# Kernel optimization log

Measured on AMD Instinct MI355X. Metric: run time of the kernel, lower is better.

## Reference

```python
import jax, jax.numpy as jnp
import numpy as np

D_MODEL = 1024
NUM_HEADS = 16
D_K = D_MODEL // NUM_HEADS  # 64


def setup_inputs() -> dict:
    key = jax.random.key(0)
    ks = jax.random.split(key, 12)
    B, S = 4, 2048
    scale = 1.0 / np.sqrt(D_MODEL)
    inp = {
        'query': jax.random.normal(ks[0], (B, S, D_MODEL), jnp.float32),
        'key': jax.random.normal(ks[1], (B, S, D_MODEL), jnp.float32),
        'value': jax.random.normal(ks[2], (B, S, D_MODEL), jnp.float32),
        # per-head projection weights stacked along head axis [H, d_model, d_k]
        'Wq': jax.random.normal(ks[3], (NUM_HEADS, D_MODEL, D_K), jnp.float32) * scale,
        'bq': jax.random.normal(ks[4], (NUM_HEADS, D_K), jnp.float32) * 0.01,
        'Wk': jax.random.normal(ks[5], (NUM_HEADS, D_MODEL, D_K), jnp.float32) * scale,
        'bk': jax.random.normal(ks[6], (NUM_HEADS, D_K), jnp.float32) * 0.01,
        'Wv': jax.random.normal(ks[7], (NUM_HEADS, D_MODEL, D_K), jnp.float32) * scale,
        'bv': jax.random.normal(ks[8], (NUM_HEADS, D_K), jnp.float32) * 0.01,
        'Wo': jax.random.normal(ks[9], (NUM_HEADS * D_K, D_MODEL), jnp.float32) * scale,
        'bo': jax.random.normal(ks[10], (D_MODEL,), jnp.float32) * 0.01,
    }
    return inp


def reference(query, key, value, Wq, bq, Wk, bk, Wv, bv, Wo, bo):
    # Per-head linear projections, batched over heads: [B,S,D] x [H,D,K] -> [B,H,S,K]
    q = jnp.einsum('bsd,hdk->bhsk', query, Wq) + bq[None, :, None, :]
    k = jnp.einsum('bsd,hdk->bhsk', key, Wk) + bk[None, :, None, :]
    v = jnp.einsum('bsd,hdk->bhsk', value, Wv) + bv[None, :, None, :]
    # Scaled dot-product attention per head
    scores = jnp.einsum('bhqk,bhsk->bhqs', q, k) / jnp.sqrt(jnp.asarray(D_K, q.dtype))
    attn = jax.nn.softmax(scores, axis=-1)
    heads = jnp.einsum('bhqs,bhsk->bhqk', attn, v)  # [B,H,S,K]
    # Concat heads -> [B,S,H*K], then output projection
    B, H, S, K = heads.shape
    concat = jnp.transpose(heads, (0, 2, 1, 3)).reshape(B, S, H * K)
    return concat @ Wo + bo
```

## Files before the change

kernel.cpp:

```cpp
#include <hip/hip_runtime.h>
#include <hip/hip_bf16.h>

typedef __bf16 bf16_t;
typedef __bf16 bf16x8 __attribute__((ext_vector_type(8)));
typedef __bf16 bf16x4 __attribute__((ext_vector_type(4)));
typedef float f32x4 __attribute__((ext_vector_type(4)));
typedef float f32x16 __attribute__((ext_vector_type(16)));

constexpr int BB = 4;
constexpr int SS = 2048;
constexpr int DM = 1024;
constexpr int NH = 16;
constexpr int DK = 64;
constexpr int MROWS = BB * SS;

template <int N> struct IC { static constexpr int V = N; };

__device__ inline uint32_t pkbf16(float a, float b) {
    union { bf16_t h[2]; uint32_t u; } x;
    x.h[0] = (bf16_t)a; x.h[1] = (bf16_t)b;
    return x.u;
}

__device__ inline float fexp2(float x) { return __builtin_amdgcn_exp2f(x); }

__device__ inline void gld16(const bf16_t* g, bf16_t* l) {
    __builtin_amdgcn_global_load_lds((const __attribute__((address_space(1))) void*)g,
                                     (__attribute__((address_space(3))) void*)l, 16, 0, 0);
}

__device__ inline f32x16 mfma32(bf16x8 a, bf16x8 b, f32x16 c) {
    return __builtin_amdgcn_mfma_f32_32x32x16_bf16(a, b, c, 0, 0, 0);
}

__device__ inline bf16x8 lds_rd(const bf16_t* base, int row, int slot) {
    return *(const bf16x8*)((const char*)base + row * 128 + ((slot ^ (row & 7)) << 4));
}

constexpr float QSCALE = (float)(1.4426950408889634 / 8.0);

__global__ __launch_bounds__(256) void k_prepw(const float* __restrict__ Wq,
                                               const float* __restrict__ Wk,
                                               const float* __restrict__ Wv,
                                               const float* __restrict__ Wo,
                                               bf16_t* __restrict__ Wt,
                                               bf16_t* __restrict__ Wot) {
    __shared__ float tile[32][33];
    const int bid = blockIdx.x;
    const int tx = threadIdx.x & 31, ty = threadIdx.x >> 5;
    if (bid < 3072) {
        const int zz = bid >> 6;
        const int r = bid & 63;
        const int cb = (r & 1) * 32, rb = (r >> 1) * 32;
        const int zt = zz >> 4, zh = zz & 15;
        const float* src = (zt == 0) ? Wq : ((zt == 1) ? Wk : Wv);
        const float sc = (zt == 0) ? QSCALE : 1.0f;
        const long zoff = (long)zh * DM * DK;
        bf16_t* d = Wt + (size_t)zt * DM * DM + (size_t)zh * DK * DM;
#pragma unroll
        for (int i = 0; i < 4; ++i) {
            int rr = rb + ty + i * 8;
            tile[ty + i * 8][tx] = src[zoff + (long)rr * DK + cb + tx];
        }
        __syncthreads();
#pragma unroll
        for (int i = 0; i < 4; ++i) {
            int c = cb + ty + i * 8;
            d[(long)c * DM + rb + tx] = (bf16_t)(tile[tx][ty + i * 8] * sc);
        }
    } else {
        const int idx = bid - 3072;
        const int cb = (idx & 31) * 32, rb = (idx >> 5) * 32;
#pragma unroll
        for (int i = 0; i < 4; ++i) {
            int rr = rb + ty + i * 8;
            tile[ty + i * 8][tx] = Wo[(long)rr * DM + cb + tx];
        }
        __syncthreads();
#pragma unroll
        for (int i = 0; i < 4; ++i) {
            int c = cb + ty + i * 8;
            Wot[(long)c * DM + rb + tx] = (bf16_t)tile[tx][ty + i * 8];
        }
    }
}

__global__ __launch_bounds__(256) void k_proj(
    const float* __restrict__ Aq, const float* __restrict__ Ak, const float* __restrict__ Av,
    const bf16_t* __restrict__ Wt,
    const float* __restrict__ bq, const float* __restrict__ bk, const float* __restrict__ bv,
    bf16_t* __restrict__ qkv) {
    const int hwid = blockIdx.x;
    const int c = hwid & 7, j = hwid >> 3;
    const int z = j >> 6;
    const int r = j & 63;
    const int n0 = (r & 7) * 128;
    const int m0 = (c * 8 + (r >> 3)) * 128;

    const float* A = (z == 0) ? Aq : ((z == 1) ? Ak : Av);
    const float* bias = (z == 0) ? bq : ((z == 1) ? bk : bv);
    const float bscale = (z == 0) ? QSCALE : 1.0f;
    const bf16_t* Bt = Wt + (size_t)z * DM * DM;
    bf16_t* outp = qkv + (size_t)z * BB * NH * SS * DK;

    __shared__ __align__(16) union SM {
        struct { bf16_t a[2][128][72]; bf16_t b[2][8192]; } s;
        bf16_t vt[128][136];
    } sm;

    const int t = threadIdx.x;
    const int lane = t & 63, w = t >> 6;
    const int lr = lane & 15, lg = lane >> 4;
    const int wr = w >> 1, wc = w & 1;

    f32x4 acc[4][4] = {};
    float4 apf[8];

    const int brow = t >> 3, bssl = t & 7;
    const size_t bsrc = (size_t)(n0 + brow) * DM + ((bssl ^ (brow & 7)) << 3);
    const int ar0 = t >> 4, aseg = t & 15;

#pragma unroll
    for (int p = 0; p < 4; ++p)
        gld16(&Bt[bsrc + p * 32 * DM], &sm.s.b[0][(p * 256 + w * 64) * 8]);
#pragma unroll
    for (int p = 0; p < 8; ++p)
        apf[p] = *(const float4*)&A[(size_t)(m0 + ar0 + p * 16) * DM + aseg * 4];
#pragma unroll
    for (int p = 0; p < 8; ++p) {
        bf16x4 pk = {(bf16_t)apf[p].x, (bf16_t)apf[p].y, (bf16_t)apf[p].z, (bf16_t)apf[p].w};
        *(bf16x4*)&sm.s.a[0][ar0 + p * 16][aseg * 4] = pk;
    }
    __syncthreads();

    auto body = [&](auto icur, int kt) {
        constexpr int cur = decltype(icur)::V;
        const int k1 = (kt + 1) * 64;
        if (kt + 1 < 16) {
#pragma unroll
            for (int p = 0; p < 4; ++p)
                gld16(&Bt[bsrc + k1 + p * 32 * DM], &sm.s.b[cur ^ 1][(p * 256 + w * 64) * 8]);
#pragma unroll
            for (int p = 0; p < 8; ++p)
                apf[p] = *(const float4*)&A[(size_t)(m0 + ar0 + p * 16) * DM + k1 + aseg * 4];
        }
#pragma unroll
        for (int ks = 0; ks < 2; ++ks) {
            const int lk = ks * 32 + lg * 8;
            bf16x8 af[4], bfm[4];
#pragma unroll
            for (int i = 0; i < 4; ++i) af[i] = *(const bf16x8*)&sm.s.a[cur][wr * 64 + i * 16 + lr][lk];
#pragma unroll
            for (int jj = 0; jj < 4; ++jj) bfm[jj] = lds_rd(sm.s.b[cur], wc * 64 + jj * 16 + lr, ks * 4 + lg);
#pragma unroll
            for (int i = 0; i < 4; ++i)
#pragma unroll
                for (int jj = 0; jj < 4; ++jj)
                    acc[i][jj] = __builtin_amdgcn_mfma_f32_16x16x32_bf16(af[i], bfm[jj], acc[i][jj], 0, 0, 0);
        }
        if (kt + 1 < 16) {
#pragma unroll
            for (int p = 0; p < 8; ++p) {
                bf16x4 pk = {(bf16_t)apf[p].x, (bf16_t)apf[p].y, (bf16_t)apf[p].z, (bf16_t)apf[p].w};
                *(bf16x4*)&sm.s.a[cur ^ 1][ar0 + p * 16][aseg * 4] = pk;
            }
        }
        __syncthreads();
    };

#pragma unroll 1
    for (int kt = 0; kt < 16; kt += 2) {
        body(IC<0>{}, kt);
        body(IC<1>{}, kt + 1);
    }

    const int b = m0 >> 11, s0 = m0 & (SS - 1);
    if (z == 2) {
#pragma unroll
        for (int i = 0; i < 4; ++i)
#pragma unroll
            for (int jj = 0; jj < 4; ++jj) {
                int col = wc * 64 + jj * 16 + lr;
                float bv_ = bias[n0 + col];
#pragma unroll
                for (int rr = 0; rr < 4; ++rr)
                    sm.vt[col][wr * 64 + i * 16 + lg * 4 + rr] = (bf16_t)(acc[i][jj][rr] + bv_);
            }
        __syncthreads();
#pragma unroll
        for (int pp = 0; pp < 8; ++pp) {
            int d = pp * 16 + (t >> 4);
            int cs = (t & 15) * 8;
            bf16x8 v = *(const bf16x8*)&sm.vt[d][cs];
            int h = (n0 + d) >> 6, dd = d & 63;
            *(bf16x8*)&outp[((size_t)(b * NH + h) * DK + dd) * SS + s0 + cs] = v;
        }
    } else {
#pragma unroll
        for (int i = 0; i < 4; ++i) {
#pragma unroll
            for (int jj = 0; jj < 4; ++jj) {
                int col = wc * 64 + jj * 16 + lr;
                int h = (n0 + col) >> 6, ko = col & 63;
                float bv_ = bias[n0 + col] * bscale;
#pragma unroll
                for (int rr = 0; rr < 4; ++rr) {
                    int s = s0 + wr * 64 + i * 16 + lg * 4 + rr;
                    outp[(((size_t)b * NH + h) * SS + s) * DK + ko] = (bf16_t)(acc[i][jj][rr] + bv_);
                }
            }
        }
    }
}

__global__ __launch_bounds__(256, 2) void k_attn(const bf16_t* __restrict__ qkv,
                                                 bf16_t* __restrict__ concat) {
    const int hw = blockIdx.x;
    const int lb = (hw & 7) * 64 + (hw >> 3);
    const int qt = lb & 7;
    const int h = (lb >> 3) & 15;
    const int b = lb >> 7;

    const size_t PH = (size_t)BB * NH * SS * DK;
    const bf16_t* qp = qkv + ((size_t)(b * NH + h) * SS) * DK;
    const bf16_t* kp = qp + PH;
    const bf16_t* vtp = qkv + 2 * PH + (size_t)(b * NH + h) * DK * SS;

    __shared__ __align__(16) bf16_t k_lds[2][4096];
    __shared__ __align__(16) bf16_t v_lds[2][4096];

    const int t = threadIdx.x;
    const int lane = t & 63, w = t >> 6;
    const int l31 = lane & 31;
    const bool hf = (lane >> 5) != 0;

    const int sr = t >> 3, ssl = t & 7;
    const int prow = (sr & ~12) | ((sr & 4) << 1) | ((sr & 8) >> 1);
    const int ssw = (ssl ^ (sr & 7)) * 8;
    const size_t okA = (size_t)prow * DK + ssw;
    const size_t ovA = (size_t)sr * SS + ssw;

    const int qbase = qt * 256 + w * 64;
    bf16x8 qf0[4], qf1[4];
#pragma unroll
    for (int ks = 0; ks < 4; ++ks) {
        qf0[ks] = *(const bf16x8*)&qp[(size_t)(qbase + l31) * DK + ks * 16 + (hf ? 8 : 0)];
        qf1[ks] = *(const bf16x8*)&qp[(size_t)(qbase + 32 + l31) * DK + ks * 16 + (hf ? 8 : 0)];
    }

    f32x16 oa00 = {}, oa01 = {}, oa10 = {}, oa11 = {};
    float lsum0 = 0.f, lsum1 = 0.f;
    f32x16 zc = {};
    asm volatile("" : "+v"(zc));

    constexpr int NT = SS / 64;

    gld16(kp + okA, &k_lds[0][w * 512]);
    gld16(kp + okA + 32 * DK, &k_lds[0][w * 512 + 2048]);
    gld16(vtp + ovA, &v_lds[0][w * 512]);
    gld16(vtp + ovA + (size_t)32 * SS, &v_lds[0][w * 512 + 2048]);
    __syncthreads();

    const bf16_t* kpp = kp + okA + 4096;
    const bf16_t* vpp = vtp + ovA + 64;

    auto body = [&](auto icur, int it) {
        constexpr int cur = decltype(icur)::V;
        if (it + 1 < NT) {
            gld16(kpp, &k_lds[cur ^ 1][w * 512]);
            gld16(kpp + 32 * DK, &k_lds[cur ^ 1][w * 512 + 2048]);
            gld16(vpp, &v_lds[cur ^ 1][w * 512]);
            gld16(vpp + (size_t)32 * SS, &v_lds[cur ^ 1][w * 512 + 2048]);
            kpp += 4096;
            vpp += 64;
        }
        f32x16 s00, s01, s10, s11;
        __builtin_amdgcn_s_setprio(1);
        {
            bf16x8 kf0 = lds_rd(k_lds[cur], l31, hf);
            bf16x8 kf1 = lds_rd(k_lds[cur], 32 + l31, hf);
            s00 = mfma32(kf0, qf0[0], zc);
            s01 = mfma32(kf1, qf0[0], zc);
            s10 = mfma32(kf0, qf1[0], zc);
            s11 = mfma32(kf1, qf1[0], zc);
        }
#pragma unroll
        for (int ks = 1; ks < 4; ++ks) {
            bf16x8 kf0 = lds_rd(k_lds[cur], l31, 2 * ks + hf);
            bf16x8 kf1 = lds_rd(k_lds[cur], 32 + l31, 2 * ks + hf);
            s00 = mfma32(kf0, qf0[ks], s00);
            s01 = mfma32(kf1, qf0[ks], s01);
            s10 = mfma32(kf0, qf1[ks], s10);
            s11 = mfma32(kf1, qf1[ks], s11);
        }
        __builtin_amdgcn_s_setprio(0);
        uint32_t wk0[16], wk1[16];
        {
            float a0 = 0.f;
#pragma unroll
            for (int pr = 0; pr < 8; ++pr) {
                float p0 = fexp2(s00[2 * pr]), p1 = fexp2(s00[2 * pr + 1]);
                a0 += p0 + p1;
                wk0[pr] = pkbf16(p0, p1);
            }
#pragma unroll
            for (int pr = 0; pr < 8; ++pr) {
                float p0 = fexp2(s01[2 * pr]), p1 = fexp2(s01[2 * pr + 1]);
                a0 += p0 + p1;
                wk0[8 + pr] = pkbf16(p0, p1);
            }
            lsum0 += a0;
            float a1 = 0.f;
#pragma unroll
            for (int pr = 0; pr < 8; ++pr) {
                float p0 = fexp2(s10[2 * pr]), p1 = fexp2(s10[2 * pr + 1]);
                a1 += p0 + p1;
                wk1[pr] = pkbf16(p0, p1);
            }
#pragma unroll
            for (int pr = 0; pr < 8; ++pr) {
                float p0 = fexp2(s11[2 * pr]), p1 = fexp2(s11[2 * pr + 1]);
                a1 += p0 + p1;
                wk1[8 + pr] = pkbf16(p0, p1);
            }
            lsum1 += a1;
        }
        __builtin_amdgcn_s_setprio(1);
#pragma unroll
        for (int kq = 0; kq < 4; ++kq) {
            bf16x8 vf0 = lds_rd(v_lds[cur], l31, 2 * kq + hf);
            bf16x8 vf1 = lds_rd(v_lds[cur], 32 + l31, 2 * kq + hf);
            union { uint32_t u[4]; bf16x8 v; } pb0, pb1;
#pragma unroll
            for (int i = 0; i < 4; ++i) { pb0.u[i] = wk0[kq * 4 + i]; pb1.u[i] = wk1[kq * 4 + i]; }
            oa00 = mfma32(vf0, pb0.v, oa00);
            oa01 = mfma32(vf1, pb0.v, oa01);
            oa10 = mfma32(vf0, pb1.v, oa10);
            oa11 = mfma32(vf1, pb1.v, oa11);
        }
        __builtin_amdgcn_s_setprio(0);
        __syncthreads();
    };

#pragma unroll 1
    for (int t2 = 0; t2 < NT; t2 += 2) {
        body(IC<0>{}, t2);
        body(IC<1>{}, t2 + 1);
    }

    {
        float l = lsum0 + __shfl_xor(lsum0, 32);
        float inv = 1.0f / l;
        const int q = qbase + l31;
#pragma unroll
        for (int dt = 0; dt < 2; ++dt) {
#pragma unroll
            for (int quad = 0; quad < 4; ++quad) {
                const f32x16& oa = dt ? oa01 : oa00;
                bf16x4 ov = {(bf16_t)(oa[quad * 4 + 0] * inv),
                             (bf16_t)(oa[quad * 4 + 1] * inv),
                             (bf16_t)(oa[quad * 4 + 2] * inv),
                             (bf16_t)(oa[quad * 4 + 3] * inv)};
                int col = dt * 32 + quad * 8 + (hf ? 4 : 0);
                *(bf16x4*)&concat[((size_t)b * SS + q) * DM + h * 64 + col] = ov;
            }
        }
    }
    {
        float l = lsum1 + __shfl_xor(lsum1, 32);
        float inv = 1.0f / l;
        const int q = qbase + 32 + l31;
#pragma unroll
        for (int dt = 0; dt < 2; ++dt) {
#pragma unroll
            for (int quad = 0; quad < 4; ++quad) {
                const f32x16& oa = dt ? oa11 : oa10;
                bf16x4 ov = {(bf16_t)(oa[quad * 4 + 0] * inv),
                             (bf16_t)(oa[quad * 4 + 1] * inv),
                             (bf16_t)(oa[quad * 4 + 2] * inv),
                             (bf16_t)(oa[quad * 4 + 3] * inv)};
                int col = dt * 32 + quad * 8 + (hf ? 4 : 0);
                *(bf16x4*)&concat[((size_t)b * SS + q) * DM + h * 64 + col] = ov;
            }
        }
    }
}

__global__ __launch_bounds__(256) void k_out(const bf16_t* __restrict__ Ab,
                                             const bf16_t* __restrict__ Wot,
                                             const float* __restrict__ bo,
                                             float* __restrict__ out) {
    const int hwid = blockIdx.x;
    const int c = hwid & 7, j = hwid >> 3;
    const int n0 = (j & 7) * 128;
    const int m0 = (c * 8 + (j >> 3)) * 128;

    __shared__ __align__(16) bf16_t a_lds[128 * 64];
    __shared__ __align__(16) bf16_t b_lds[128 * 64];

    const int t = threadIdx.x;
    const int lane = t & 63, w = t >> 6;
    const int lr = lane & 15, lg = lane >> 4;
    const int wr = w >> 1, wc = w & 1;

    f32x4 acc[4][4] = {};

    for (int kt = 0; kt < 16; ++kt) {
        const int k0 = kt * 64;
#pragma unroll
        for (int p = 0; p < 4; ++p) {
            int id = p * 256 + t;
            int row = id >> 3, ssl = id & 7;
            int sc = (ssl ^ (row & 7)) << 3;
            gld16(&Ab[(size_t)(m0 + row) * DM + k0 + sc], a_lds + (size_t)(p * 256 + w * 64) * 8);
            gld16(&Wot[(size_t)(n0 + row) * DM + k0 + sc], b_lds + (size_t)(p * 256 + w * 64) * 8);
        }
        __syncthreads();
#pragma unroll
        for (int ks = 0; ks < 2; ++ks) {
            bf16x8 af[4], bfm[4];
#pragma unroll
            for (int i = 0; i < 4; ++i) af[i] = lds_rd(a_lds, wr * 64 + i * 16 + lr, ks * 4 + lg);
#pragma unroll
            for (int jj = 0; jj < 4; ++jj) bfm[jj] = lds_rd(b_lds, wc * 64 + jj * 16 + lr, ks * 4 + lg);
#pragma unroll
            for (int i = 0; i < 4; ++i)
#pragma unroll
                for (int jj = 0; jj < 4; ++jj)
                    acc[i][jj] = __builtin_amdgcn_mfma_f32_16x16x32_bf16(af[i], bfm[jj], acc[i][jj], 0, 0, 0);
        }
        __syncthreads();
    }
#pragma unroll
    for (int i = 0; i < 4; ++i) {
#pragma unroll
        for (int jj = 0; jj < 4; ++jj) {
            int col = n0 + wc * 64 + jj * 16 + lr;
            float bv_ = bo[col];
#pragma unroll
            for (int rr = 0; rr < 4; ++rr) {
                int mrow = m0 + wr * 64 + i * 16 + lg * 4 + rr;
                out[(size_t)mrow * DM + col] = acc[i][jj][rr] + bv_;
            }
        }
    }
}

extern "C" void kernel_launch(void* const* d_in, const int* in_sizes, int n_in,
                              void* d_out, int out_size, void* d_ws, size_t ws_size,
                              hipStream_t stream) {
    const float* query = (const float*)d_in[0];
    const float* key   = (const float*)d_in[1];
    const float* value = (const float*)d_in[2];
    const float* Wq = (const float*)d_in[3];
    const float* bq = (const float*)d_in[4];
    const float* Wk = (const float*)d_in[5];
    const float* bk = (const float*)d_in[6];
    const float* Wv = (const float*)d_in[7];
    const float* bv = (const float*)d_in[8];
    const float* Wo = (const float*)d_in[9];
    const float* bo = (const float*)d_in[10];

    char* ws = (char*)d_ws;
    bf16_t* qkv    = (bf16_t*)ws;
    bf16_t* Wt     = (bf16_t*)(ws + (size_t)50331648);
    bf16_t* Wot    = (bf16_t*)(ws + (size_t)56623104);
    bf16_t* concat = (bf16_t*)(ws + (size_t)58720256);

    k_prepw<<<dim3(4096), 256, 0, stream>>>(Wq, Wk, Wv, Wo, Wt, Wot);
    k_proj<<<dim3(1536), 256, 0, stream>>>(query, key, value, Wt, bq, bk, bv, qkv);
    k_attn<<<dim3(512), 256, 0, stream>>>(qkv, concat);
    k_out<<<dim3(512), 256, 0, stream>>>(concat, Wot, bo, (float*)d_out);
}
```

Measured before the change: 188.3 us.

## Pre-convert activations to bf16 and load both GEMM operands via direct-to-LDS

```diff
diff --git a/kernel.cpp b/kernel.cpp
--- a/kernel.cpp
+++ b/kernel.cpp
@@ -39,18 +39,36 @@
 
 constexpr float QSCALE = (float)(1.4426950408889634 / 8.0);
 
-__global__ __launch_bounds__(256) void k_prepw(const float* __restrict__ Wq,
-                                               const float* __restrict__ Wk,
-                                               const float* __restrict__ Wv,
-                                               const float* __restrict__ Wo,
-                                               bf16_t* __restrict__ Wt,
-                                               bf16_t* __restrict__ Wot) {
+__global__ __launch_bounds__(256) void k_prep(const float* __restrict__ Aq,
+                                              const float* __restrict__ Ak,
+                                              const float* __restrict__ Av,
+                                              const float* __restrict__ Wq,
+                                              const float* __restrict__ Wk,
+                                              const float* __restrict__ Wv,
+                                              const float* __restrict__ Wo,
+                                              bf16_t* __restrict__ Ab,
+                                              bf16_t* __restrict__ Wt,
+                                              bf16_t* __restrict__ Wot) {
+    const int bid = blockIdx.x;
+    if (bid < 2048) {
+        for (size_t g = (size_t)bid * 256 + threadIdx.x; g < 3145728; g += 2048 * 256) {
+            const size_t zi = g >> 20;
+            const size_t off = (g & 1048575) * 8;
+            const float* src = (zi == 0) ? Aq : ((zi == 1) ? Ak : Av);
+            float4 a = *(const float4*)&src[off];
+            float4 b = *(const float4*)&src[off + 4];
+            bf16x8 o = {(bf16_t)a.x, (bf16_t)a.y, (bf16_t)a.z, (bf16_t)a.w,
+                        (bf16_t)b.x, (bf16_t)b.y, (bf16_t)b.z, (bf16_t)b.w};
+            *(bf16x8*)&Ab[g * 8] = o;
+        }
+        return;
+    }
     __shared__ float tile[32][33];
-    const int bid = blockIdx.x;
     const int tx = threadIdx.x & 31, ty = threadIdx.x >> 5;
-    if (bid < 3072) {
-        const int zz = bid >> 6;
-        const int r = bid & 63;
+    if (bid < 5120) {
+        const int idx = bid - 2048;
+        const int zz = idx >> 6;
+        const int r = idx & 63;
         const int cb = (r & 1) * 32, rb = (r >> 1) * 32;
         const int zt = zz >> 4, zh = zz & 15;
         const float* src = (zt == 0) ? Wq : ((zt == 1) ? Wk : Wv);
@@ -69,7 +87,7 @@
             d[(long)c * DM + rb + tx] = (bf16_t)(tile[tx][ty + i * 8] * sc);
         }
     } else {
-        const int idx = bid - 3072;
+        const int idx = bid - 5120;
         const int cb = (idx & 31) * 32, rb = (idx >> 5) * 32;
 #pragma unroll
         for (int i = 0; i < 4; ++i) {
@@ -86,8 +104,7 @@
 }
 
 __global__ __launch_bounds__(256) void k_proj(
-    const float* __restrict__ Aq, const float* __restrict__ Ak, const float* __restrict__ Av,
-    const bf16_t* __restrict__ Wt,
+    const bf16_t* __restrict__ Ab3, const bf16_t* __restrict__ Wt,
     const float* __restrict__ bq, const float* __restrict__ bk, const float* __restrict__ bv,
     bf16_t* __restrict__ qkv) {
     const int hwid = blockIdx.x;
@@ -97,14 +114,14 @@
     const int n0 = (r & 7) * 128;
     const int m0 = (c * 8 + (r >> 3)) * 128;
 
-    const float* A = (z == 0) ? Aq : ((z == 1) ? Ak : Av);
+    const bf16_t* A = Ab3 + (size_t)z * MROWS * DM;
     const float* bias = (z == 0) ? bq : ((z == 1) ? bk : bv);
     const float bscale = (z == 0) ? QSCALE : 1.0f;
     const bf16_t* Bt = Wt + (size_t)z * DM * DM;
     bf16_t* outp = qkv + (size_t)z * BB * NH * SS * DK;
 
     __shared__ __align__(16) union SM {
-        struct { bf16_t a[2][128][72]; bf16_t b[2][8192]; } s;
+        struct { bf16_t a[128 * 64]; bf16_t b[128 * 64]; } s;
         bf16_t vt[128][136];
     } sm;
 
@@ -114,66 +131,33 @@
     const int wr = w >> 1, wc = w & 1;
 
     f32x4 acc[4][4] = {};
-    float4 apf[8];
-
-    const int brow = t >> 3, bssl = t & 7;
-    const size_t bsrc = (size_t)(n0 + brow) * DM + ((bssl ^ (brow & 7)) << 3);
-    const int ar0 = t >> 4, aseg = t & 15;
-
-#pragma unroll
-    for (int p = 0; p < 4; ++p)
-        gld16(&Bt[bsrc + p * 32 * DM], &sm.s.b[0][(p * 256 + w * 64) * 8]);
-#pragma unroll
-    for (int p = 0; p < 8; ++p)
-        apf[p] = *(const float4*)&A[(size_t)(m0 + ar0 + p * 16) * DM + aseg * 4];
-#pragma unroll
-    for (int p = 0; p < 8; ++p) {
-        bf16x4 pk = {(bf16_t)apf[p].x, (bf16_t)apf[p].y, (bf16_t)apf[p].z, (bf16_t)apf[p].w};
-        *(bf16x4*)&sm.s.a[0][ar0 + p * 16][aseg * 4] = pk;
-    }
-    __syncthreads();
-
-    auto body = [&](auto icur, int kt) {
-        constexpr int cur = decltype(icur)::V;
-        const int k1 = (kt + 1) * 64;
-        if (kt + 1 < 16) {
-#pragma unroll
-            for (int p = 0; p < 4; ++p)
-                gld16(&Bt[bsrc + k1 + p * 32 * DM], &sm.s.b[cur ^ 1][(p * 256 + w * 64) * 8]);
-#pragma unroll
-            for (int p = 0; p < 8; ++p)
-                apf[p] = *(const float4*)&A[(size_t)(m0 + ar0 + p * 16) * DM + k1 + aseg * 4];
-        }
+
+    for (int kt = 0; kt < 16; ++kt) {
+        const int k0 = kt * 64;
+#pragma unroll
+        for (int p = 0; p < 4; ++p) {
+            int id = p * 256 + t;
+            int rw = id >> 3, sl = id & 7;
+            int sc = (sl ^ (rw & 7)) << 3;
+            gld16(&A[(size_t)(m0 + rw) * DM + k0 + sc], sm.s.a + (size_t)(p * 256 + w * 64) * 8);
+            gld16(&Bt[(size_t)(n0 + rw) * DM + k0 + sc], sm.s.b + (size_t)(p * 256 + w * 64) * 8);
+        }
+        __syncthreads();
 #pragma unroll
         for (int ks = 0; ks < 2; ++ks) {
-            const int lk = ks * 32 + lg * 8;
             bf16x8 af[4], bfm[4];
 #pragma unroll
-            for (int i = 0; i < 4; ++i) af[i] = *(const bf16x8*)&sm.s.a[cur][wr * 64 + i * 16 + lr][lk];
-#pragma unroll
-            for (int jj = 0; jj < 4; ++jj) bfm[jj] = lds_rd(sm.s.b[cur], wc * 64 + jj * 16 + lr, ks * 4 + lg);
+            for (int i = 0; i < 4; ++i) af[i] = lds_rd(sm.s.a, wr * 64 + i * 16 + lr, ks * 4 + lg);
+#pragma unroll
+            for (int jj = 0; jj < 4; ++jj) bfm[jj] = lds_rd(sm.s.b, wc * 64 + jj * 16 + lr, ks * 4 + lg);
 #pragma unroll
             for (int i = 0; i < 4; ++i)
 #pragma unroll
                 for (int jj = 0; jj < 4; ++jj)
                     acc[i][jj] = __builtin_amdgcn_mfma_f32_16x16x32_bf16(af[i], bfm[jj], acc[i][jj], 0, 0, 0);
         }
-        if (kt + 1 < 16) {
-#pragma unroll
-            for (int p = 0; p < 8; ++p) {
-                bf16x4 pk = {(bf16_t)apf[p].x, (bf16_t)apf[p].y, (bf16_t)apf[p].z, (bf16_t)apf[p].w};
-                *(bf16x4*)&sm.s.a[cur ^ 1][ar0 + p * 16][aseg * 4] = pk;
-            }
-        }
-        __syncthreads();
-    };
-
-#pragma unroll 1
-    for (int kt = 0; kt < 16; kt += 2) {
-        body(IC<0>{}, kt);
-        body(IC<1>{}, kt + 1);
-    }
-
+        __syncthreads();
+    }
     const int b = m0 >> 11, s0 = m0 & (SS - 1);
     if (z == 2) {
 #pragma unroll
@@ -465,10 +449,11 @@
     bf16_t* qkv    = (bf16_t*)ws;
     bf16_t* Wt     = (bf16_t*)(ws + (size_t)50331648);
     bf16_t* Wot    = (bf16_t*)(ws + (size_t)56623104);
+    bf16_t* Ab     = (bf16_t*)(ws + (size_t)58720256);
     bf16_t* concat = (bf16_t*)(ws + (size_t)58720256);
 
-    k_prepw<<<dim3(4096), 256, 0, stream>>>(Wq, Wk, Wv, Wo, Wt, Wot);
-    k_proj<<<dim3(1536), 256, 0, stream>>>(query, key, value, Wt, bq, bk, bv, qkv);
+    k_prep<<<dim3(6144), 256, 0, stream>>>(query, key, value, Wq, Wk, Wv, Wo, Ab, Wt, Wot);
+    k_proj<<<dim3(1536), 256, 0, stream>>>(Ab, Wt, bq, bk, bv, qkv);
     k_attn<<<dim3(512), 256, 0, stream>>>(qkv, concat);
     k_out<<<dim3(512), 256, 0, stream>>>(concat, Wot, bo, (float*)d_out);
 }
```

Result: slower. 198.2 us (+5.3%).
